# Performance work log

Hardware: AMD Instinct MI355X
Metric: run time of the kernel (lower is better)

Reference implementation:

```python
import jax, jax.numpy as jnp
import numpy as np
import math

EPS = 1e-5
L2_EPS = 1e-12  # torch F.normalize default eps


def _bitlinear(x, W):
    """BitNet b1.58-style BitLinear: ternary weights (per-tensor mean-abs scale)
    and per-token int8 absmax activation quantization. No bias.
    x: [..., in], W: [out, in] -> [..., out]
    """
    w_scale = jnp.clip(jnp.mean(jnp.abs(W)), EPS, None)
    W_q = jnp.clip(jnp.round(W / w_scale), -1.0, 1.0) * w_scale
    x_scale = 127.0 / jnp.clip(jnp.max(jnp.abs(x), axis=-1, keepdims=True), EPS, None)
    x_q = jnp.clip(jnp.round(x * x_scale), -128.0, 127.0) / x_scale
    return jnp.einsum('bsi,oi->bso', x_q, W_q)


def setup_inputs() -> dict:
    key = jax.random.key(0)
    k1, k2, k3 = jax.random.split(key, 3)
    B, S, D_in, P, D_out = 4, 4096, 2048, 16, 2048
    x = jax.random.normal(k1, (B, S, D_in), dtype=jnp.float32)
    # xavier_normal_: std = sqrt(2 / (fan_in + fan_out))
    Wk = jax.random.normal(k2, (P, D_in), dtype=jnp.float32) * math.sqrt(2.0 / (D_in + P))
    Wv = jax.random.normal(k3, (D_out, P), dtype=jnp.float32) * math.sqrt(2.0 / (P + D_out))
    return {"x": x, "Wk": Wk, "Wv": Wv}


def reference(x, Wk, Wv):
    # key projection -> [B, S, P]
    attn = _bitlinear(x, Wk)
    # gelu (exact erf form, torch default) + L2-normalize * sqrt(P)
    attn = jax.nn.gelu(attn, approximate=False)
    norm = jnp.clip(jnp.linalg.norm(attn, axis=-1, keepdims=True), L2_EPS, None)
    attn = attn / norm * jnp.sqrt(jnp.float32(attn.shape[-1]))
    # value projection -> [B, S, D_out]
    return _bitlinear(attn, Wv)
```

## Files before the change

### kernel.cpp

```cpp
#include <hip/hip_runtime.h>
#include <hip/hip_bf16.h>

#define DIN   2048
#define DOUT  2048
#define NP    16
#define TPW   8

#define HDR_OFF   0
#define WK4_OFF   16
#define WV4_OFF   (WK4_OFF + 32768)
#define Q2_OFF    (WV4_OFF + 32768)

static __device__ __forceinline__ int dot4(unsigned a, unsigned b, int c) {
#if defined(__has_builtin) && __has_builtin(__builtin_amdgcn_sdot4)
  return __builtin_amdgcn_sdot4((int)a, (int)b, c, false);
#else
  c += (int)(signed char)(a & 0xffu)        * (int)(signed char)(b & 0xffu);
  c += (int)(signed char)((a >> 8) & 0xffu) * (int)(signed char)((b >> 8) & 0xffu);
  c += (int)(signed char)((a >> 16) & 0xffu)* (int)(signed char)((b >> 16) & 0xffu);
  c += (int)(signed char)(a >> 24)          * (int)(signed char)(b >> 24);
  return c;
#endif
}

static __device__ __forceinline__ unsigned q8(float f, float xs) {
  float t = f * xs;
  float r = rintf(t);
  r = fmaxf(-128.0f, fminf(127.0f, r));
  return ((unsigned)(int)r) & 0xffu;
}

__global__ __launch_bounds__(256) void prep_kernel(
    const float* __restrict__ Wk, const float* __restrict__ Wv,
    float* __restrict__ hdr, unsigned* __restrict__ wk4, unsigned* __restrict__ wv4)
{
  __shared__ float red[256];
  __shared__ float s_scale;
  const int tid = threadIdx.x;
  const float* W = (blockIdx.x == 0) ? Wk : Wv;

  float s = 0.f;
  for (int i = 0; i < 128; ++i) s += fabsf(W[tid + i * 256]);
  red[tid] = s;
  __syncthreads();
  for (int o = 128; o > 0; o >>= 1) {
    if (tid < o) red[tid] += red[tid + o];
    __syncthreads();
  }
  if (tid == 0) {
    float sc = fmaxf(red[0] * (1.0f / 32768.0f), 1e-5f);
    s_scale = sc;
    hdr[blockIdx.x] = sc;
  }
  __syncthreads();
  const float sc = s_scale;

  if (blockIdx.x == 0) {
    for (int i = 0; i < 32; ++i) {
      int c = tid + i * 256;
      unsigned pk = 0;
#pragma unroll
      for (int j = 0; j < 4; ++j) {
        float r = rintf(W[c * 4 + j] / sc);
        r = fmaxf(-1.0f, fminf(1.0f, r));
        pk |= (((unsigned)(int)r) & 0xffu) << (8 * j);
      }
      wk4[c] = pk;
    }
  } else {
    for (int i = 0; i < 8; ++i) {
      int o = tid + i * 256;
      unsigned u[4];
#pragma unroll
      for (int c = 0; c < 4; ++c) {
        unsigned pk = 0;
#pragma unroll
        for (int r = 0; r < 4; ++r) {
          float q = rintf(W[o * 16 + c * 4 + r] / sc);
          q = fmaxf(-1.0f, fminf(1.0f, q));
          pk |= (((unsigned)(int)q) & 0xffu) << (8 * r);
        }
        u[c] = pk;
      }
      ((uint4*)wv4)[o] = make_uint4(u[0], u[1], u[2], u[3]);
    }
  }
}

__global__ __launch_bounds__(64, 2) void kA(
    const float* __restrict__ x, const float* __restrict__ hdr,
    const unsigned* __restrict__ wk4, uint4* __restrict__ q2w, float* __restrict__ s2w)
{
  const int l = threadIdx.x;
  const long t0 = (long)blockIdx.x * TPW;
  const float w1 = hdr[0], w2 = hdr[1];

  unsigned wk[16][8];
#pragma unroll
  for (int p = 0; p < 16; ++p)
#pragma unroll
    for (int c = 0; c < 8; ++c) wk[p][c] = wk4[p * 512 + c * 64 + l];

  const float4* xf = (const float4*)x;

  for (int i = 0; i < TPW; ++i) {
    const long tok = t0 + i;

    float4 a[8];
#pragma unroll
    for (int c = 0; c < 8; ++c) a[c] = xf[tok * 512 + c * 64 + l];

    float mx = 0.0f;
#pragma unroll
    for (int c = 0; c < 8; ++c) {
      mx = fmaxf(mx, fabsf(a[c].x)); mx = fmaxf(mx, fabsf(a[c].y));
      mx = fmaxf(mx, fabsf(a[c].z)); mx = fmaxf(mx, fabsf(a[c].w));
    }
#pragma unroll
    for (int d = 1; d < 64; d <<= 1) mx = fmaxf(mx, __shfl_xor(mx, d, 64));
    const float mcl = fmaxf(mx, 1e-5f);
    const float xs = 127.0f / mcl;
    const float s1 = w1 / xs;

    unsigned qp[8];
#pragma unroll
    for (int c = 0; c < 8; ++c) {
      qp[c] = q8(a[c].x, xs) | (q8(a[c].y, xs) << 8)
            | (q8(a[c].z, xs) << 16) | (q8(a[c].w, xs) << 24);
    }

    int acc[16];
#pragma unroll
    for (int p = 0; p < 16; ++p) {
      int d = 0;
#pragma unroll
      for (int c = 0; c < 8; ++c) d = dot4(qp[c], wk[p][c], d);
      acc[p] = d;
    }

#pragma unroll
    for (int p = 0; p < 16; ++p) {
#pragma unroll
      for (int d = 1; d < 64; d <<= 1) acc[p] += __shfl_xor(acc[p], d, 64);
    }

    float g[16];
    float ss = 0.0f;
#pragma unroll
    for (int p = 0; p < 16; ++p) {
      float fa = (float)acc[p] * s1;
      float gv = 0.5f * fa * (1.0f + erff(fa * 0.70710678118654752f));
      g[p] = gv;
      ss += gv * gv;
    }
    float rn = fmaxf(sqrtf(ss), 1e-12f);
    float inv = 4.0f / rn;
    float am = 0.0f;
#pragma unroll
    for (int p = 0; p < 16; ++p) {
      g[p] *= inv;
      am = fmaxf(am, fabsf(g[p]));
    }
    const float mc2 = fmaxf(am, 1e-5f);
    const float xs2 = 127.0f / mc2;
    const float s2 = w2 / xs2;

    unsigned wq[4] = {0u, 0u, 0u, 0u};
#pragma unroll
    for (int p = 0; p < 16; ++p) wq[p >> 2] |= q8(g[p], xs2) << ((p & 3) * 8);

    if (l == 0) {
      q2w[tok] = make_uint4(wq[0], wq[1], wq[2], wq[3]);
      s2w[tok] = s2;
    }
  }
}

__global__ __launch_bounds__(64, 2) void kB(
    const uint4* __restrict__ wv4, const uint4* __restrict__ q2w,
    const float* __restrict__ s2w, float* __restrict__ out)
{
  const int l = threadIdx.x;
  const long t0 = (long)blockIdx.x * TPW;

  uint4 wv[8][4];
#pragma unroll
  for (int m = 0; m < 8; ++m)
#pragma unroll
    for (int j = 0; j < 4; ++j) wv[m][j] = wv4[m * 256 + l * 4 + j];

  for (int i = 0; i < TPW; ++i) {
    const long tok = t0 + i;
    const uint4 q = q2w[tok];
    const float s2 = s2w[tok];
#pragma unroll
    for (int m = 0; m < 8; ++m) {
      float h[4];
#pragma unroll
      for (int j = 0; j < 4; ++j) {
        int d = dot4(q.x, wv[m][j].x, 0);
        d = dot4(q.y, wv[m][j].y, d);
        d = dot4(q.z, wv[m][j].z, d);
        d = dot4(q.w, wv[m][j].w, d);
        h[j] = (float)d * s2;
      }
      *(float4*)(out + (size_t)tok * 2048 + m * 256 + l * 4) =
          make_float4(h[0], h[1], h[2], h[3]);
    }
  }
}

extern "C" void kernel_launch(void* const* d_in, const int* in_sizes, int n_in,
                              void* d_out, int out_size, void* d_ws, size_t ws_size,
                              hipStream_t stream) {
  const float* x  = (const float*)d_in[0];
  const float* Wk = (const float*)d_in[1];
  const float* Wv = (const float*)d_in[2];

  const int tokens = in_sizes[0] / DIN;

  char* ws = (char*)d_ws;
  float*    hdr = (float*)(ws + HDR_OFF);
  unsigned* wk4 = (unsigned*)(ws + WK4_OFF);
  unsigned* wv4 = (unsigned*)(ws + WV4_OFF);
  uint4*    q2w = (uint4*)(ws + Q2_OFF);
  float*    s2w = (float*)(ws + Q2_OFF + (size_t)tokens * 16);

  prep_kernel<<<2, 256, 0, stream>>>(Wk, Wv, hdr, wk4, wv4);
  kA<<<tokens / TPW, 64, 0, stream>>>(x, hdr, wk4, q2w, s2w);
  kB<<<tokens / TPW, 64, 0, stream>>>((const uint4*)wv4, q2w, s2w, (float*)d_out);
}
```

Measured before the change: 267.1 us.

## Parallelize weight prep, use transpose-style shuffle reduction and magic-number quantization

Weight preparation is split from a 2-block kernel into a 16-block partial-sum reduction followed by a 40-block packing kernel, so it no longer runs on just two workgroups. In kA, the 16 per-projection wave reductions (16x6 shuffles) become a butterfly transpose-reduce that leaves one projection per lane. Four tokens' epilogues (GELU, L2 norm, requantization) are then handled in parallel across 16-lane groups. Activation quantization uses a fused multiply-add with the 1.5*2^23 constant plus a byte mask instead of rint, clamp and convert. This drops the explicit clamp, which is safe only because absmax scaling keeps values within ±127. It adds an extra kernel launch.

Measured after the change: 254.4 us. -4.7%, faster.

```diff
diff --git a/kernel.cpp b/kernel.cpp
--- a/kernel.cpp
+++ b/kernel.cpp
@@ -7,7 +7,8 @@
 #define TPW   8
 
 #define HDR_OFF   0
-#define WK4_OFF   16
+#define PART_OFF  64
+#define WK4_OFF   256
 #define WV4_OFF   (WK4_OFF + 32768)
 #define Q2_OFF    (WV4_OFF + 32768)
 
@@ -23,6 +24,10 @@
 #endif
 }
 
+static __device__ __forceinline__ unsigned qmagic(float f, float xs) {
+  return __float_as_uint(fmaf(f, xs, 12582912.0f)) & 0xffu;
+}
+
 static __device__ __forceinline__ unsigned q8(float f, float xs) {
   float t = f * xs;
   float r = rintf(t);
@@ -30,60 +35,72 @@
   return ((unsigned)(int)r) & 0xffu;
 }
 
-__global__ __launch_bounds__(256) void prep_kernel(
+__global__ __launch_bounds__(256) void k_reduce(
     const float* __restrict__ Wk, const float* __restrict__ Wv,
-    float* __restrict__ hdr, unsigned* __restrict__ wk4, unsigned* __restrict__ wv4)
+    float* __restrict__ partials)
 {
   __shared__ float red[256];
-  __shared__ float s_scale;
-  const int tid = threadIdx.x;
-  const float* W = (blockIdx.x == 0) ? Wk : Wv;
+  const int tid = threadIdx.x, b = blockIdx.x;
+  const float4* W = (const float4*)((b < 8) ? Wk : Wv);
+  const int lb = b & 7;
 
   float s = 0.f;
-  for (int i = 0; i < 128; ++i) s += fabsf(W[tid + i * 256]);
+#pragma unroll
+  for (int i = 0; i < 4; ++i) {
+    float4 v = W[lb * 1024 + i * 256 + tid];
+    s += fabsf(v.x) + fabsf(v.y) + fabsf(v.z) + fabsf(v.w);
+  }
   red[tid] = s;
   __syncthreads();
   for (int o = 128; o > 0; o >>= 1) {
     if (tid < o) red[tid] += red[tid + o];
     __syncthreads();
   }
-  if (tid == 0) {
-    float sc = fmaxf(red[0] * (1.0f / 32768.0f), 1e-5f);
-    s_scale = sc;
-    hdr[blockIdx.x] = sc;
-  }
-  __syncthreads();
-  const float sc = s_scale;
-
-  if (blockIdx.x == 0) {
-    for (int i = 0; i < 32; ++i) {
-      int c = tid + i * 256;
+  if (tid == 0) partials[b] = red[0];
+}
+
+__global__ __launch_bounds__(256) void k_pack(
+    const float* __restrict__ Wk, const float* __restrict__ Wv,
+    const float* __restrict__ partials, float* __restrict__ hdr,
+    unsigned* __restrict__ wk4, unsigned* __restrict__ wv4)
+{
+  const int tid = threadIdx.x, b = blockIdx.x;
+  const int isV = (b >= 32);
+  float sum = 0.f;
+#pragma unroll
+  for (int i = 0; i < 8; ++i) sum += partials[isV * 8 + i];
+  const float sc = fmaxf(sum * (1.0f / 32768.0f), 1e-5f);
+  if (tid == 0 && (b == 0 || b == 32)) hdr[isV] = sc;
+
+  if (!isV) {
+    const int c = b * 256 + tid;
+    float4 w = ((const float4*)Wk)[c];
+    unsigned pk = 0;
+    const float* wp = &w.x;
+#pragma unroll
+    for (int j = 0; j < 4; ++j) {
+      float r = rintf(wp[j] / sc);
+      r = fmaxf(-1.0f, fminf(1.0f, r));
+      pk |= (((unsigned)(int)r) & 0xffu) << (8 * j);
+    }
+    wk4[c] = pk;
+  } else {
+    const int o = (b - 32) * 256 + tid;
+    unsigned u[4];
+#pragma unroll
+    for (int c = 0; c < 4; ++c) {
+      float4 w = ((const float4*)Wv)[o * 4 + c];
+      const float* wp = &w.x;
       unsigned pk = 0;
 #pragma unroll
-      for (int j = 0; j < 4; ++j) {
-        float r = rintf(W[c * 4 + j] / sc);
-        r = fmaxf(-1.0f, fminf(1.0f, r));
-        pk |= (((unsigned)(int)r) & 0xffu) << (8 * j);
-      }
-      wk4[c] = pk;
-    }
-  } else {
-    for (int i = 0; i < 8; ++i) {
-      int o = tid + i * 256;
-      unsigned u[4];
-#pragma unroll
-      for (int c = 0; c < 4; ++c) {
-        unsigned pk = 0;
-#pragma unroll
-        for (int r = 0; r < 4; ++r) {
-          float q = rintf(W[o * 16 + c * 4 + r] / sc);
-          q = fmaxf(-1.0f, fminf(1.0f, q));
-          pk |= (((unsigned)(int)q) & 0xffu) << (8 * r);
-        }
-        u[c] = pk;
-      }
-      ((uint4*)wv4)[o] = make_uint4(u[0], u[1], u[2], u[3]);
-    }
+      for (int r = 0; r < 4; ++r) {
+        float q = rintf(wp[r] / sc);
+        q = fmaxf(-1.0f, fminf(1.0f, q));
+        pk |= (((unsigned)(int)q) & 0xffu) << (8 * r);
+      }
+      u[c] = pk;
+    }
+    ((uint4*)wv4)[o] = make_uint4(u[0], u[1], u[2], u[3]);
   }
 }
 
@@ -103,6 +120,9 @@
 
   const float4* xf = (const float4*)x;
 
+  int   svi[4];
+  float s1v[4];
+
   for (int i = 0; i < TPW; ++i) {
     const long tok = t0 + i;
 
@@ -120,13 +140,13 @@
     for (int d = 1; d < 64; d <<= 1) mx = fmaxf(mx, __shfl_xor(mx, d, 64));
     const float mcl = fmaxf(mx, 1e-5f);
     const float xs = 127.0f / mcl;
-    const float s1 = w1 / xs;
+    s1v[i & 3] = w1 / xs;
 
     unsigned qp[8];
 #pragma unroll
     for (int c = 0; c < 8; ++c) {
-      qp[c] = q8(a[c].x, xs) | (q8(a[c].y, xs) << 8)
-            | (q8(a[c].z, xs) << 16) | (q8(a[c].w, xs) << 24);
+      qp[c] = qmagic(a[c].x, xs) | (qmagic(a[c].y, xs) << 8)
+            | (qmagic(a[c].z, xs) << 16) | (qmagic(a[c].w, xs) << 24);
     }
 
     int acc[16];
@@ -139,39 +159,58 @@
     }
 
 #pragma unroll
-    for (int p = 0; p < 16; ++p) {
-#pragma unroll
-      for (int d = 1; d < 64; d <<= 1) acc[p] += __shfl_xor(acc[p], d, 64);
-    }
-
-    float g[16];
-    float ss = 0.0f;
-#pragma unroll
-    for (int p = 0; p < 16; ++p) {
-      float fa = (float)acc[p] * s1;
-      float gv = 0.5f * fa * (1.0f + erff(fa * 0.70710678118654752f));
-      g[p] = gv;
-      ss += gv * gv;
-    }
-    float rn = fmaxf(sqrtf(ss), 1e-12f);
-    float inv = 4.0f / rn;
-    float am = 0.0f;
-#pragma unroll
-    for (int p = 0; p < 16; ++p) {
-      g[p] *= inv;
-      am = fmaxf(am, fabsf(g[p]));
-    }
-    const float mc2 = fmaxf(am, 1e-5f);
-    const float xs2 = 127.0f / mc2;
-    const float s2 = w2 / xs2;
-
-    unsigned wq[4] = {0u, 0u, 0u, 0u};
-#pragma unroll
-    for (int p = 0; p < 16; ++p) wq[p >> 2] |= q8(g[p], xs2) << ((p & 3) * 8);
-
-    if (l == 0) {
-      q2w[tok] = make_uint4(wq[0], wq[1], wq[2], wq[3]);
-      s2w[tok] = s2;
+    for (int b = 0; b < 4; ++b) {
+      const int lb = (l >> b) & 1;
+#pragma unroll
+      for (int j = 0; j < 8; ++j) {
+        if (j < (8 >> b)) {
+          int keep = lb ? acc[2 * j + 1] : acc[2 * j];
+          int send = lb ? acc[2 * j]     : acc[2 * j + 1];
+          acc[j] = keep + __shfl_xor(send, 1 << b, 64);
+        }
+      }
+    }
+    svi[i & 3] = acc[0];
+
+    if ((i & 3) == 3) {
+      const int lb4 = (l >> 4) & 1, lb5 = (l >> 5) & 1;
+      int r0 = (lb4 ? svi[1] : svi[0]) + __shfl_xor(lb4 ? svi[0] : svi[1], 16, 64);
+      int r1 = (lb4 ? svi[3] : svi[2]) + __shfl_xor(lb4 ? svi[2] : svi[3], 16, 64);
+      int rr = (lb5 ? r1 : r0) + __shfl_xor(lb5 ? r0 : r1, 32, 64);
+      float s1a = lb4 ? s1v[1] : s1v[0];
+      float s1b = lb4 ? s1v[3] : s1v[2];
+      const float s1sel = lb5 ? s1b : s1a;
+
+      const float fa = (float)rr * s1sel;
+      const float gv = 0.5f * fa * (1.0f + erff(fa * 0.70710678118654752f));
+      float ss = gv * gv;
+      ss += __shfl_xor(ss, 1, 64); ss += __shfl_xor(ss, 2, 64);
+      ss += __shfl_xor(ss, 4, 64); ss += __shfl_xor(ss, 8, 64);
+      const float rn = fmaxf(sqrtf(ss), 1e-12f);
+      const float gn = gv * (4.0f / rn);
+      float am = fabsf(gn);
+      {
+        float o;
+        o = __shfl_xor(am, 1, 64); am = fmaxf(am, o);
+        o = __shfl_xor(am, 2, 64); am = fmaxf(am, o);
+        o = __shfl_xor(am, 4, 64); am = fmaxf(am, o);
+        o = __shfl_xor(am, 8, 64); am = fmaxf(am, o);
+      }
+      const float mc2 = fmaxf(am, 1e-5f);
+      const float xs2 = 127.0f / mc2;
+      const float s2 = w2 / xs2;
+
+      unsigned sh = q8(gn, xs2) << ((l & 3) * 8);
+      sh |= (unsigned)__shfl_xor((int)sh, 1, 64);
+      sh |= (unsigned)__shfl_xor((int)sh, 2, 64);
+      const unsigned wa = (unsigned)__shfl_xor((int)sh, 4, 64);
+      const unsigned wb = (unsigned)__shfl_xor((int)sh, 8, 64);
+      const unsigned wc = (unsigned)__shfl_xor((int)sh, 12, 64);
+      if ((l & 15) == 0) {
+        const long tk = t0 + (i & ~3) + (l >> 4);
+        q2w[tk] = make_uint4(sh, wa, wb, wc);
+        s2w[tk] = s2;
+      }
     }
   }
 }
@@ -220,13 +259,15 @@
   const int tokens = in_sizes[0] / DIN;
 
   char* ws = (char*)d_ws;
-  float*    hdr = (float*)(ws + HDR_OFF);
-  unsigned* wk4 = (unsigned*)(ws + WK4_OFF);
-  unsigned* wv4 = (unsigned*)(ws + WV4_OFF);
-  uint4*    q2w = (uint4*)(ws + Q2_OFF);
-  float*    s2w = (float*)(ws + Q2_OFF + (size_t)tokens * 16);
-
-  prep_kernel<<<2, 256, 0, stream>>>(Wk, Wv, hdr, wk4, wv4);
+  float*    hdr  = (float*)(ws + HDR_OFF);
+  float*    part = (float*)(ws + PART_OFF);
+  unsigned* wk4  = (unsigned*)(ws + WK4_OFF);
+  unsigned* wv4  = (unsigned*)(ws + WV4_OFF);
+  uint4*    q2w  = (uint4*)(ws + Q2_OFF);
+  float*    s2w  = (float*)(ws + Q2_OFF + (size_t)tokens * 16);
+
+  k_reduce<<<16, 256, 0, stream>>>(Wk, Wv, part);
+  k_pack<<<40, 256, 0, stream>>>(Wk, Wv, part, hdr, wk4, wv4);
   kA<<<tokens / TPW, 64, 0, stream>>>(x, hdr, wk4, q2w, s2w);
   kB<<<tokens / TPW, 64, 0, stream>>>((const uint4*)wv4, q2w, s2w, (float*)d_out);
 }
```
